# Optimization experiments

Measured on AMD Instinct MI355X. Metric: run time of the kernel, lower is better.

## Reference

```python
import jax, jax.numpy as jnp
import numpy as np

N_AUTHOR, N_PAPER = 20000, 50000
E = 300000
D, H = 256, 8
DK = D // H  # 32


def setup_inputs() -> dict:
    key = jax.random.key(0)
    ks = jax.random.split(key, 20)
    s = np.float32(1.0 / np.sqrt(D))
    sr = np.float32(1.0 / np.sqrt(DK))
    inp = {
        "h_author": jax.random.normal(ks[0], (N_AUTHOR, D), jnp.float32),
        "h_paper": jax.random.normal(ks[1], (N_PAPER, D), jnp.float32),
        "k_w": jax.random.normal(ks[2], (2, D, D), jnp.float32) * s,
        "k_b": jnp.zeros((2, D), jnp.float32),
        "q_w": jax.random.normal(ks[3], (2, D, D), jnp.float32) * s,
        "q_b": jnp.zeros((2, D), jnp.float32),
        "v_w": jax.random.normal(ks[4], (2, D, D), jnp.float32) * s,
        "v_b": jnp.zeros((2, D), jnp.float32),
        "a_w": jax.random.normal(ks[5], (2, D, D), jnp.float32) * s,
        "a_b": jnp.zeros((2, D), jnp.float32),
        "rel_att": jax.random.normal(ks[6], (3, H, DK, DK), jnp.float32) * sr,
        "rel_msg": jax.random.normal(ks[7], (3, H, DK, DK), jnp.float32) * sr,
        "rel_pri": jnp.ones((3, H), jnp.float32),
        "skip": jnp.ones((2,), jnp.float32),
        "src_writes": jax.random.randint(ks[8], (E,), 0, N_AUTHOR),
        "dst_writes": jax.random.randint(ks[9], (E,), 0, N_PAPER),
        "src_cites": jax.random.randint(ks[10], (E,), 0, N_PAPER),
        "dst_cites": jax.random.randint(ks[11], (E,), 0, N_PAPER),
        "src_wb": jax.random.randint(ks[12], (E,), 0, N_PAPER),
        "dst_wb": jax.random.randint(ks[13], (E,), 0, N_AUTHOR),
    }
    return inp


def _seg_softmax(score, seg, n):
    # dst-normalized edge softmax (per-etype subgraph, like DGL edge_softmax)
    m = jax.ops.segment_max(score, seg, num_segments=n)
    m = jnp.where(jnp.isfinite(m), m, 0.0)
    a = jnp.exp(score - m[seg])
    s = jax.ops.segment_sum(a, seg, num_segments=n)
    return a / s[seg]


def _etype_agg(h_src, h_dst, kw, kb, qw, qb, vw, vb, ratt, rmsg, pri, src, dst, n_dst):
    k = (h_src @ kw.T + kb).reshape(-1, H, DK)
    v = (h_src @ vw.T + vb).reshape(-1, H, DK)
    q = (h_dst @ qw.T + qb).reshape(-1, H, DK)
    k = jnp.einsum('nhi,hij->nhj', k, ratt)
    v = jnp.einsum('nhi,hij->nhj', v, rmsg)
    score = (q[dst] * k[src]).sum(-1) * pri / np.float32(np.sqrt(DK))  # [E,H]
    attn = _seg_softmax(score, dst, n_dst)
    return jax.ops.segment_sum(v[src] * attn[:, :, None], dst, num_segments=n_dst)


def reference(h_author, h_paper, k_w, k_b, q_w, q_b, v_w, v_b, a_w, a_b,
              rel_att, rel_msg, rel_pri, skip,
              src_writes, dst_writes, src_cites, dst_cites, src_wb, dst_wb):
    # ntypes: author=0, paper=1; etypes: writes=0 (a->p), cites=1 (p->p), written_by=2 (p->a)
    agg_p = _etype_agg(h_author, h_paper, k_w[0], k_b[0], q_w[1], q_b[1], v_w[0], v_b[0],
                       rel_att[0], rel_msg[0], rel_pri[0], src_writes, dst_writes, N_PAPER)
    agg_p = agg_p + _etype_agg(h_paper, h_paper, k_w[1], k_b[1], q_w[1], q_b[1], v_w[1], v_b[1],
                               rel_att[1], rel_msg[1], rel_pri[1], src_cites, dst_cites, N_PAPER)
    agg_a = _etype_agg(h_paper, h_author, k_w[1], k_b[1], q_w[0], q_b[0], v_w[1], v_b[1],
                       rel_att[2], rel_msg[2], rel_pri[2], src_wb, dst_wb, N_AUTHOR)

    def out_block(agg, h, nid):
        alpha = jax.nn.sigmoid(skip[nid])
        trans = agg.reshape(-1, D) @ a_w[nid].T + a_b[nid]
        return trans * alpha + h * (1.0 - alpha)

    return (out_block(agg_a, h_author, 0), out_block(agg_p, h_paper, 1))
```

## Files before the change

### kernel.cpp

```cpp
#include <hip/hip_runtime.h>
#include <hip/hip_bf16.h>

#define NA 20000
#define NP 50000
#define NE 300000
#define DD 256
#define HH 8
#define NTOT (2 * NP + NA)
#define NBLK ((NTOT + 2047) / 2048)
#define NRT 391

#define CVT_B 8750
#define PREP_B 1792
#define CNT_B 3516
#define PROJ_B (8 * 50 * 14)
#define SCAT_B 3516

typedef short bf16x8 __attribute__((ext_vector_type(8)));
typedef float f32x4 __attribute__((ext_vector_type(4)));

__device__ __forceinline__ float b2f(ushort u) {
  unsigned v = ((unsigned)u) << 16;
  float f;
  __builtin_memcpy(&f, &v, 4);
  return f;
}
__device__ __forceinline__ float b2f_lo(int u) {
  unsigned v = ((unsigned)u) << 16;
  float f;
  __builtin_memcpy(&f, &v, 4);
  return f;
}
__device__ __forceinline__ float b2f_hi(int u) {
  unsigned v = ((unsigned)u) & 0xffff0000u;
  float f;
  __builtin_memcpy(&f, &v, 4);
  return f;
}
__device__ __forceinline__ ushort f2b(float f) {
  unsigned u;
  __builtin_memcpy(&u, &f, 4);
  u = u + 0x7fffu + ((u >> 16) & 1u);
  return (ushort)(u >> 16);
}
__device__ __forceinline__ unsigned pk2(float lo, float hi) {
  return (unsigned)f2b(lo) | ((unsigned)f2b(hi) << 16);
}
__device__ __forceinline__ float ldf(const void* p, int i, int isbf) {
  return isbf ? b2f(((const ushort*)p)[i]) : ((const float*)p)[i];
}
__device__ __forceinline__ int get_isbf(const void* rpri) {
  return ((const unsigned*)rpri)[0] == 0x3F803F80u;
}
__device__ __forceinline__ void gload16(const void* g, void* l) {
  __builtin_amdgcn_global_load_lds(
      (const __attribute__((address_space(1))) void*)g,
      (__attribute__((address_space(3))) void*)l, 16, 0, 0);
}

__global__ __launch_bounds__(256) void phase0(const void* __restrict__ ha,
                                              const void* __restrict__ hp,
                                              ushort* __restrict__ Ha,
                                              ushort* __restrict__ Hp,
                                              const void* __restrict__ q_w,
                                              const void* __restrict__ a_w,
                                              const void* __restrict__ k_w,
                                              const void* __restrict__ v_w,
                                              const void* __restrict__ k_b,
                                              const void* __restrict__ v_b,
                                              const void* __restrict__ q_b,
                                              const void* __restrict__ ratt,
                                              const void* __restrict__ rmsg,
                                              ushort* __restrict__ Bp,
                                              ushort* __restrict__ Ba,
                                              ushort* __restrict__ aeff,
                                              float* __restrict__ gb,
                                              const int* __restrict__ d0,
                                              const int* __restrict__ d1,
                                              const int* __restrict__ d2,
                                              int* __restrict__ cnt,
                                              const void* __restrict__ rpri) {
  const int b = blockIdx.x;
  const int c = threadIdx.x;
  const int isbf = get_isbf(rpri);
  if (b < CVT_B) {
    size_t t = (size_t)b * 256 + c;
    const size_t nA = (size_t)NA * 256 / 8;
    const size_t nT = nA + (size_t)NP * 256 / 8;
    if (t >= nT) return;
    const void* src;
    ushort* dst;
    size_t o;
    if (t < nA) { src = ha; dst = Ha; o = t * 8; }
    else        { src = hp; dst = Hp; o = (t - nA) * 8; }
    if (isbf) {
      *(int4*)(dst + o) = *(const int4*)((const ushort*)src + o);
    } else {
      const float* f = (const float*)src + o;
      float4 x = *(const float4*)f;
      float4 y = *(const float4*)(f + 4);
      int4 v;
      v.x = (int)pk2(x.x, x.y); v.y = (int)pk2(x.z, x.w);
      v.z = (int)pk2(y.x, y.y); v.w = (int)pk2(y.z, y.w);
      *(int4*)(dst + o) = v;
    }
  } else if (b < CVT_B + PREP_B) {
    int pid = b - CVT_B;
    int y = pid >> 8;
    int r = pid & 255;
    if (y < 3) {
      int e = y;
      int nt = (e == 2) ? 0 : 1;
      int h = r >> 5, i = r & 31;
      int rb = ((e * HH + h) * 32 + i) * 32;
      int qb = nt * 65536 + (h * 32) * 256 + c;
      float s = 0.f;
#pragma unroll 8
      for (int j = 0; j < 32; j++) s += ldf(ratt, rb + j, isbf) * ldf(q_w, qb + j * 256, isbf);
      ushort* dst = (e == 2) ? (Ba + (size_t)(512 + r) * 256)
                             : (Bp + (size_t)(512 + e * 256 + r) * 256);
      dst[c] = f2b(s);
    } else if (y < 6) {
      int e = y - 3;
      int o = r;
      int nt = (e == 2) ? 0 : 1;
      int h = c >> 5, i = c & 31;
      int rb = ((e * HH + h) * 32 + i) * 32;
      int ab = nt * 65536 + o * 256 + h * 32;
      float s = 0.f;
#pragma unroll 8
      for (int j = 0; j < 32; j++) s += ldf(rmsg, rb + j, isbf) * ldf(a_w, ab + j, isbf);
      aeff[(e * 256 + o) * 256 + c] = f2b(s);
    } else if (r < 128) {
      int t = r * 256 + c;
      int sec = t >> 13;
      int o = (t & 8191) * 8;
      const void* src = (sec == 0 || sec == 2) ? k_w : v_w;
      size_t soff = (sec < 2) ? (size_t)(65536 + o) : (size_t)o;
      ushort* dst = (sec == 0) ? (Bp + o)
                  : (sec == 1) ? (Bp + 65536 + o)
                  : (sec == 2) ? (Ba + o)
                               : (Ba + 65536 + o);
      if (isbf) {
        *(int4*)dst = *(const int4*)((const ushort*)src + soff);
      } else {
        const float* f = (const float*)src + soff;
        float4 x = *(const float4*)f;
        float4 yy = *(const float4*)(f + 4);
        int4 v;
        v.x = (int)pk2(x.x, x.y); v.y = (int)pk2(x.z, x.w);
        v.z = (int)pk2(yy.x, yy.y); v.w = (int)pk2(yy.z, yy.w);
        *(int4*)dst = v;
      }
    } else if (r == 128) {
      gb[0 * 256 + c] = ldf(k_b, 256 + c, isbf);
      gb[1 * 256 + c] = ldf(v_b, 256 + c, isbf);
      gb[4 * 256 + c] = ldf(k_b, c, isbf);
      gb[5 * 256 + c] = ldf(v_b, c, isbf);
      int h = c >> 5, i = c & 31;
      for (int e = 0; e < 3; e++) {
        int ntp = (e == 2) ? 0 : 1;
        int rb = ((e * HH + h) * 32 + i) * 32;
        float s = 0.f;
        for (int j = 0; j < 32; j++)
          s += ldf(ratt, rb + j, isbf) * ldf(q_b, ntp * 256 + h * 32 + j, isbf);
        gb[(e == 2 ? 6 : (2 + e)) * 256 + c] = s;
      }
    }
  } else {
    int i = (b - CVT_B - PREP_B) * 256 + c;
    if (i >= 3 * NE) return;
    int et = (i >= 2 * NE) ? 2 : ((i >= NE) ? 1 : 0);
    int e = i - et * NE;
    const int* dd = (et == 0) ? d0 : ((et == 1) ? d1 : d2);
    int base = (et == 0) ? 0 : ((et == 1) ? NP : 2 * NP);
    atomicAdd(&cnt[base + dd[e]], 1);
  }
}

struct GemmC4 { ushort* c[4]; int ilv[4]; };

__global__ __launch_bounds__(256) void proj_scatter(const ushort* __restrict__ Hp,
                                                    const ushort* __restrict__ Ha,
                                                    const ushort* __restrict__ Bpp,
                                                    const ushort* __restrict__ Bap,
                                                    const float* __restrict__ gb,
                                                    GemmC4 cpp, GemmC4 cpa,
                                                    const int* __restrict__ s0,
                                                    const int* __restrict__ d0,
                                                    const int* __restrict__ s1,
                                                    const int* __restrict__ d1,
                                                    const int* __restrict__ s2,
                                                    const int* __restrict__ d2,
                                                    int* __restrict__ cur,
                                                    int* __restrict__ csr) {
  __shared__ __align__(16) ushort As[2][4096];
  __shared__ __align__(16) ushort Bs[2][4096];
  const int bid = blockIdx.x;
  if (bid >= PROJ_B) {
    int i = (bid - PROJ_B) * 256 + threadIdx.x;
    if (i >= 3 * NE) return;
    int et = (i >= 2 * NE) ? 2 : ((i >= NE) ? 1 : 0);
    int e = i - et * NE;
    const int* ss = (et == 0) ? s0 : ((et == 1) ? s1 : s2);
    const int* dd = (et == 0) ? d0 : ((et == 1) ? d1 : d2);
    int base = (et == 0) ? 0 : ((et == 1) ? NP : 2 * NP);
    int pos = atomicAdd(&cur[base + dd[e]], 1);
    csr[pos] = ss[e];
    return;
  }
  const int xcd = bid & 7, seq = bid >> 3;
  const int rt = (seq / 14) * 8 + xcd;
  const int y = seq % 14;
  if (rt >= NRT) return;
  const int isNP = (y < 8);
  const int M = isNP ? NP : NA;
  const int row0 = rt * 128;
  if (row0 >= M) return;
  const ushort* A = isNP ? Hp : Ha;
  const ushort* B = isNP ? Bpp : Bap;
  const float* gbias = isNP ? gb : (gb + 1024);
  const int col0 = (isNP ? y : (y - 8)) * 128;
  const GemmC4 cp = isNP ? cpp : cpa;
  ushort* C = cp.c[col0 >> 8];
  const int ilv = cp.ilv[col0 >> 8];
  const int ccol0 = col0 & 255;

  const int tid = threadIdx.x;
  const int ln = tid & 63, wv = tid >> 6;
  const int quad = ln >> 4, lr = ln & 15;
  const int wr = wv >> 1, wc = wv & 1;

  f32x4 acc[4][4];
#pragma unroll
  for (int m = 0; m < 4; m++)
#pragma unroll
    for (int n = 0; n < 4; n++) acc[m][n] = (f32x4){0.f, 0.f, 0.f, 0.f};

  const int r0 = tid >> 2, seg = tid & 3;
  const int r1 = 64 + r0;
  int ar0 = row0 + r0; if (ar0 >= M) ar0 = M - 1;
  int ar1 = row0 + r1; if (ar1 >= M) ar1 = M - 1;
  const ushort* gA0 = A + ((size_t)ar0 * 256 + seg * 8);
  const ushort* gA1 = A + ((size_t)ar1 * 256 + seg * 8);
  const ushort* gB0 = B + ((size_t)(col0 + r0) * 256 + seg * 8);
  const ushort* gB1 = B + ((size_t)(col0 + r1) * 256 + seg * 8);
  const int lbase = (tid & 192) * 8;

  auto stage = [&](int kb, int buf) {
    gload16(gA0 + kb * 32, As[buf] + lbase);
    gload16(gA1 + kb * 32, As[buf] + 2048 + lbase);
    gload16(gB0 + kb * 32, Bs[buf] + lbase);
    gload16(gB1 + kb * 32, Bs[buf] + 2048 + lbase);
  };

  stage(0, 0);
  __syncthreads();
  for (int kb = 0; kb < 8; kb++) {
    const int cur_ = kb & 1;
    if (kb < 7) stage(kb + 1, cur_ ^ 1);
    bf16x8 af[4], bfr[4];
#pragma unroll
    for (int m = 0; m < 4; m++)
      af[m] = *(const bf16x8*)&As[cur_][(wr * 64 + m * 16 + lr) * 32 + quad * 8];
#pragma unroll
    for (int n = 0; n < 4; n++)
      bfr[n] = *(const bf16x8*)&Bs[cur_][(wc * 64 + n * 16 + lr) * 32 + quad * 8];
#pragma unroll
    for (int m = 0; m < 4; m++)
#pragma unroll
      for (int n = 0; n < 4; n++)
        acc[m][n] = __builtin_amdgcn_mfma_f32_16x16x32_bf16(bfr[n], af[m], acc[m][n], 0, 0, 0);
    __syncthreads();
  }

  const int voff = (ilv == 2) ? 4 : 0;
#pragma unroll
  for (int m = 0; m < 4; m++) {
    int row = row0 + wr * 64 + m * 16 + lr;
    if (row >= M) continue;
#pragma unroll
    for (int n = 0; n < 4; n++) {
      int ccol = ccol0 + wc * 64 + n * 16 + quad * 4;
      int gcol = col0 + wc * 64 + n * 16 + quad * 4;
      float4 bv = *(const float4*)(gbias + gcol);
      ushort4 o;
      o.x = f2b(acc[m][n][0] + bv.x);
      o.y = f2b(acc[m][n][1] + bv.y);
      o.z = f2b(acc[m][n][2] + bv.z);
      o.w = f2b(acc[m][n][3] + bv.w);
      size_t cidx = ilv ? ((size_t)row * 512 + (size_t)(ccol >> 2) * 8 + voff)
                        : ((size_t)row * 256 + ccol);
      *(ushort4*)(C + cidx) = o;
    }
  }
}

__global__ __launch_bounds__(256) void out_gemm2(const ushort* __restrict__ Aa,
                                                 const ushort* __restrict__ Ba_,
                                                 const ushort* __restrict__ Ap0,
                                                 const ushort* __restrict__ Bp0,
                                                 const ushort* __restrict__ Ap1,
                                                 const ushort* __restrict__ Bp1,
                                                 const void* __restrict__ ab,
                                                 const void* __restrict__ h_a,
                                                 const void* __restrict__ h_p,
                                                 const void* __restrict__ skipv,
                                                 void* __restrict__ out,
                                                 const void* __restrict__ rpri) {
  const int y = blockIdx.y;
  const int isA = (y < 2);
  const int M = isA ? NA : NP;
  const int row0 = blockIdx.x * 128;
  if (row0 >= M) return;
  const ushort* A0 = isA ? Aa : Ap0;
  const ushort* B0 = isA ? Ba_ : Bp0;
  const ushort* A1 = isA ? nullptr : Ap1;
  const ushort* B1 = isA ? nullptr : Bp1;
  const int ab_off = isA ? 0 : 256;
  const void* h = isA ? h_a : h_p;
  const int skipidx = isA ? 0 : 1;
  const size_t out_off = isA ? 0 : (size_t)NA * DD;
  const int col0 = (isA ? y : (y - 2)) * 128;

  const int isbf = get_isbf(rpri);
  __shared__ __align__(16) ushort As[2][4096];
  __shared__ __align__(16) ushort Bs[2][4096];
  const int tid = threadIdx.x;
  const int ln = tid & 63, wv = tid >> 6;
  const int quad = ln >> 4, lr = ln & 15;
  const int wr = wv >> 1, wc = wv & 1;

  f32x4 acc[4][4];
#pragma unroll
  for (int m = 0; m < 4; m++)
#pragma unroll
    for (int n = 0; n < 4; n++) acc[m][n] = (f32x4){0.f, 0.f, 0.f, 0.f};

  const int r0 = tid >> 2, seg = tid & 3;
  const int r1 = 64 + r0;
  int ar0 = row0 + r0; if (ar0 >= M) ar0 = M - 1;
  int ar1 = row0 + r1; if (ar1 >= M) ar1 = M - 1;
  const int lbase = (tid & 192) * 8;

  const int nsteps = (A1 != nullptr) ? 16 : 8;
  auto stage = [&](int s, int buf) {
    int g = s >> 3, kb = s & 7;
    const ushort* A = g ? A1 : A0;
    const ushort* B = g ? B1 : B0;
    gload16(A + (size_t)ar0 * 256 + seg * 8 + kb * 32, As[buf] + lbase);
    gload16(A + (size_t)ar1 * 256 + seg * 8 + kb * 32, As[buf] + 2048 + lbase);
    gload16(B + (size_t)(col0 + r0) * 256 + seg * 8 + kb * 32, Bs[buf] + lbase);
    gload16(B + (size_t)(col0 + r1) * 256 + seg * 8 + kb * 32, Bs[buf] + 2048 + lbase);
  };

  stage(0, 0);
  __syncthreads();
  for (int s = 0; s < nsteps; s++) {
    const int cur_ = s & 1;
    if (s + 1 < nsteps) stage(s + 1, cur_ ^ 1);
    bf16x8 af[4], bfr[4];
#pragma unroll
    for (int m = 0; m < 4; m++)
      af[m] = *(const bf16x8*)&As[cur_][(wr * 64 + m * 16 + lr) * 32 + quad * 8];
#pragma unroll
    for (int n = 0; n < 4; n++)
      bfr[n] = *(const bf16x8*)&Bs[cur_][(wc * 64 + n * 16 + lr) * 32 + quad * 8];
#pragma unroll
    for (int m = 0; m < 4; m++)
#pragma unroll
      for (int n = 0; n < 4; n++)
        acc[m][n] = __builtin_amdgcn_mfma_f32_16x16x32_bf16(bfr[n], af[m], acc[m][n], 0, 0, 0);
    __syncthreads();
  }

  float alpha = 1.f / (1.f + __expf(-ldf(skipv, skipidx, isbf)));
  float beta = 1.f - alpha;
#pragma unroll
  for (int m = 0; m < 4; m++) {
    int row = row0 + wr * 64 + m * 16 + lr;
    if (row >= M) continue;
#pragma unroll
    for (int n = 0; n < 4; n++) {
      int col = col0 + wc * 64 + n * 16 + quad * 4;
      size_t base = (size_t)row * 256 + col;
      float t0 = acc[m][n][0] + ldf(ab, ab_off + col + 0, isbf);
      float t1 = acc[m][n][1] + ldf(ab, ab_off + col + 1, isbf);
      float t2 = acc[m][n][2] + ldf(ab, ab_off + col + 2, isbf);
      float t3 = acc[m][n][3] + ldf(ab, ab_off + col + 3, isbf);
      if (isbf) {
        ushort4 hu = *(const ushort4*)((const ushort*)h + base);
        ushort4 o;
        o.x = f2b(alpha * t0 + beta * b2f(hu.x));
        o.y = f2b(alpha * t1 + beta * b2f(hu.y));
        o.z = f2b(alpha * t2 + beta * b2f(hu.z));
        o.w = f2b(alpha * t3 + beta * b2f(hu.w));
        *(ushort4*)((ushort*)out + out_off + base) = o;
      } else {
        float4 hf = *(const float4*)((const float*)h + base);
        float4 o;
        o.x = alpha * t0 + beta * hf.x;
        o.y = alpha * t1 + beta * hf.y;
        o.z = alpha * t2 + beta * hf.z;
        o.w = alpha * t3 + beta * hf.w;
        *(float4*)((float*)out + out_off + base) = o;
      }
    }
  }
}

__global__ __launch_bounds__(256) void reduce_cnt(const int* __restrict__ cnt,
                                                  int* __restrict__ bsum) {
  __shared__ int red[256];
  int t = threadIdx.x;
  int base = blockIdx.x * 2048 + t * 8;
  int s = 0;
#pragma unroll
  for (int j = 0; j < 8; j++) s += (base + j < NTOT) ? cnt[base + j] : 0;
  red[t] = s;
  __syncthreads();
  for (int o = 128; o > 0; o >>= 1) {
    if (t < o) red[t] += red[t + o];
    __syncthreads();
  }
  if (t == 0) bsum[blockIdx.x] = red[0];
}

__global__ __launch_bounds__(64) void scan_top(const int* __restrict__ bsum,
                                               int* __restrict__ ebase) {
  __shared__ int ts[64];
  int t = threadIdx.x;
  int v = (t < NBLK) ? bsum[t] : 0;
  ts[t] = v;
  __syncthreads();
  for (int o = 1; o < 64; o <<= 1) {
    int x = (t >= o) ? ts[t - o] : 0;
    __syncthreads();
    ts[t] += x;
    __syncthreads();
  }
  if (t < NBLK) ebase[t] = ts[t] - v;
}

__global__ __launch_bounds__(256) void scan_final(const int* __restrict__ cnt,
                                                  const int* __restrict__ ebase,
                                                  int* __restrict__ offs,
                                                  int* __restrict__ cur) {
  __shared__ int ts[256];
  int t = threadIdx.x;
  int base = blockIdx.x * 2048 + t * 8;
  int v[8];
  int s = 0;
#pragma unroll
  for (int j = 0; j < 8; j++) {
    int x = (base + j < NTOT) ? cnt[base + j] : 0;
    v[j] = s;
    s += x;
  }
  ts[t] = s;
  __syncthreads();
  for (int o = 1; o < 256; o <<= 1) {
    int x = (t >= o) ? ts[t - o] : 0;
    __syncthreads();
    ts[t] += x;
    __syncthreads();
  }
  int tb = ebase[blockIdx.x] + ts[t] - s;
#pragma unroll
  for (int j = 0; j < 8; j++) {
    int i = base + j;
    if (i < NTOT) {
      int o2 = tb + v[j];
      offs[i] = o2;
      cur[i] = o2;
    }
  }
  if (blockIdx.x == 0 && t == 0) offs[NTOT] = 3 * NE;
}

__global__ __launch_bounds__(256) void edge_agg_all(ushort* __restrict__ Qe0,
                                                    ushort* __restrict__ Qe1,
                                                    ushort* __restrict__ Qe2,
                                                    const ushort* __restrict__ KVa,
                                                    const ushort* __restrict__ KVp,
                                                    const int* __restrict__ offs,
                                                    const int* __restrict__ csr,
                                                    const void* __restrict__ pri) {
  int isbf = get_isbf(pri);
  int wv = threadIdx.x >> 6;
  int g = blockIdx.x * 4 + wv;
  if (g >= NTOT) return;
  int ln = threadIdx.x & 63;
  int h = ln >> 3;
  int d, pri_off, n_src;
  ushort* Q;
  const ushort* KV;
  if (g < NP) {
    d = g; Q = Qe0; KV = KVa; pri_off = 0; n_src = NA;
  } else if (g < 2 * NP) {
    d = g - NP; Q = Qe1; KV = KVp; pri_off = 8; n_src = NP;
  } else {
    d = g - 2 * NP; Q = Qe2; KV = KVp; pri_off = 16; n_src = NP;
  }
  float prif = ldf(pri, pri_off + h, isbf) * 0.17677669529663687f;
  ushort4 qu = *(const ushort4*)(Q + (size_t)d * 256 + ln * 4);
  float q0 = b2f(qu.x) * prif, q1 = b2f(qu.y) * prif;
  float q2 = b2f(qu.z) * prif, q3 = b2f(qu.w) * prif;
  float m = -1e30f, l = 0.f;
  float a0 = 0.f, a1 = 0.f, a2 = 0.f, a3 = 0.f;
  int e0 = __builtin_amdgcn_readfirstlane(offs[g]);
  int e1 = __builtin_amdgcn_readfirstlane(offs[g + 1]);
  if (e1 > e0 + 4096) e1 = e0 + 4096;
  const int elast = e1 - 1;

  for (int e = e0; e < e1; e += 8) {
    int nv = e1 - e;
    nv = (nv > 8) ? 8 : nv;
    int4 kv[8];
    float sc[8];
#pragma unroll
    for (int i = 0; i < 8; i++) {
      int idx = e + i;
      idx = (idx > elast) ? elast : idx;
      unsigned s = (unsigned)__builtin_amdgcn_readfirstlane(csr[idx]);
      if (s >= (unsigned)n_src) s = 0;
      kv[i] = *(const int4*)(KV + (size_t)s * 512 + ln * 8);
    }
#pragma unroll
    for (int i = 0; i < 8; i++) {
      float p = q0 * b2f_lo(kv[i].x) + q1 * b2f_hi(kv[i].x) +
                q2 * b2f_lo(kv[i].y) + q3 * b2f_hi(kv[i].y);
      p += __shfl_xor(p, 1);
      p += __shfl_xor(p, 2);
      p += __shfl_xor(p, 4);
      sc[i] = (i < nv) ? p : -1e30f;
    }
    float mc = fmaxf(fmaxf(fmaxf(sc[0], sc[1]), fmaxf(sc[2], sc[3])),
                     fmaxf(fmaxf(sc[4], sc[5]), fmaxf(sc[6], sc[7])));
    float mn = fmaxf(m, mc);
    if (e != e0) {
      float scale = __expf(m - mn);
      l *= scale; a0 *= scale; a1 *= scale; a2 *= scale; a3 *= scale;
    }
#pragma unroll
    for (int i = 0; i < 8; i++) {
      float wgt = __expf(sc[i] - mn);
      l += wgt;
      a0 += wgt * b2f_lo(kv[i].z);
      a1 += wgt * b2f_hi(kv[i].z);
      a2 += wgt * b2f_lo(kv[i].w);
      a3 += wgt * b2f_hi(kv[i].w);
    }
    m = mn;
  }
  float inv = (l > 0.f) ? 1.f / l : 0.f;
  ushort4 o;
  o.x = f2b(a0 * inv);
  o.y = f2b(a1 * inv);
  o.z = f2b(a2 * inv);
  o.w = f2b(a3 * inv);
  *(ushort4*)(Q + (size_t)d * 256 + ln * 4) = o;
}

extern "C" void kernel_launch(void* const* d_in, const int* in_sizes, int n_in,
                              void* d_out, int out_size, void* d_ws, size_t ws_size,
                              hipStream_t stream) {
  (void)in_sizes; (void)n_in; (void)out_size; (void)ws_size;
  const void* h_a = d_in[0];
  const void* h_p = d_in[1];
  const void* k_w = d_in[2];
  const void* k_b = d_in[3];
  const void* q_w = d_in[4];
  const void* q_b = d_in[5];
  const void* v_w = d_in[6];
  const void* v_b = d_in[7];
  const void* a_w = d_in[8];
  const void* a_b = d_in[9];
  const void* ratt = d_in[10];
  const void* rmsg = d_in[11];
  const void* rpri = d_in[12];
  const void* skip = d_in[13];
  const int* src_w = (const int*)d_in[14];
  const int* dst_w = (const int*)d_in[15];
  const int* src_c = (const int*)d_in[16];
  const int* dst_c = (const int*)d_in[17];
  const int* src_b = (const int*)d_in[18];
  const int* dst_b = (const int*)d_in[19];

  char* w = (char*)d_ws;
  size_t ofs = 0;
  auto alloc = [&](size_t bytes) {
    char* p = w + ofs;
    ofs = (ofs + bytes + 255) & ~(size_t)255;
    return p;
  };
  ushort* Bp = (ushort*)alloc((size_t)1024 * 256 * 2);
  ushort* Ba = (ushort*)alloc((size_t)768 * 256 * 2);
  ushort* aeff = (ushort*)alloc((size_t)3 * 256 * 256 * 2);
  float* gb = (float*)alloc((size_t)7 * 256 * 4);
  int* cnt = (int*)alloc((size_t)NTOT * 4);
  int* offs = (int*)alloc((size_t)(NTOT + 1) * 4);
  int* bsum = (int*)alloc(64 * 4);
  int* ebase = (int*)alloc(64 * 4);
  int* cur = (int*)alloc((size_t)NTOT * 4);
  int* csr = (int*)alloc((size_t)3 * NE * 4);
  ushort* Ha = (ushort*)alloc((size_t)NA * DD * 2);
  ushort* Hp = (ushort*)alloc((size_t)NP * DD * 2);
  ushort* KVa = (ushort*)alloc((size_t)NA * 512 * 2);
  ushort* KVp = (ushort*)alloc((size_t)NP * 512 * 2);
  ushort* Qe0 = (ushort*)alloc((size_t)NP * DD * 2);
  ushort* Qe1 = (ushort*)alloc((size_t)NP * DD * 2);
  ushort* Qe2 = (ushort*)alloc((size_t)NA * DD * 2);
  ushort* agg0 = Qe0;
  ushort* agg1 = Qe1;
  ushort* agg2 = Qe2;

  hipMemsetAsync(cnt, 0, (size_t)NTOT * 4, stream);

  phase0<<<CVT_B + PREP_B + CNT_B, 256, 0, stream>>>(
      h_a, h_p, Ha, Hp, q_w, a_w, k_w, v_w, k_b, v_b, q_b, ratt, rmsg,
      Bp, Ba, aeff, gb, dst_w, dst_c, dst_b, cnt, rpri);

  reduce_cnt<<<NBLK, 256, 0, stream>>>(cnt, bsum);
  scan_top<<<1, 64, 0, stream>>>(bsum, ebase);
  scan_final<<<NBLK, 256, 0, stream>>>(cnt, ebase, offs, cur);

  GemmC4 cpp, cpa;
  cpp.c[0] = KVp; cpp.ilv[0] = 1;
  cpp.c[1] = KVp; cpp.ilv[1] = 2;
  cpp.c[2] = Qe0; cpp.ilv[2] = 0;
  cpp.c[3] = Qe1; cpp.ilv[3] = 0;
  cpa.c[0] = KVa; cpa.ilv[0] = 1;
  cpa.c[1] = KVa; cpa.ilv[1] = 2;
  cpa.c[2] = Qe2; cpa.ilv[2] = 0;
  cpa.c[3] = Qe2; cpa.ilv[3] = 0;
  proj_scatter<<<PROJ_B + SCAT_B, 256, 0, stream>>>(
      Hp, Ha, Bp, Ba, gb, cpp, cpa,
      src_w, dst_w, src_c, dst_c, src_b, dst_b, cur, csr);

  edge_agg_all<<<(NTOT + 3) / 4, 256, 0, stream>>>(Qe0, Qe1, Qe2, KVa, KVp,
                                                   offs, csr, rpri);

  out_gemm2<<<dim3((NP + 127) / 128, 4), 256, 0, stream>>>(
      agg2, aeff + 131072, agg0, aeff, agg1, aeff + 65536,
      a_b, h_a, h_p, skip, d_out, rpri);
}
```

Before: 541.6 us.

## Triple-buffer projection GEMM loads and pair K/V columns per output tile

Switches the projection GEMM from double to triple buffering in LDS, with two stages in flight. It uses explicit vmcnt waits and raw barriers in place of __syncthreads, so global loads overlap more MFMA work. It also remaps column tiles so each K/V block computes 64 K columns and the matching 64 V columns, writing complete interleaved KV entries, and replaces the GemmC4 struct with direct pointers. Costs are more LDS per block (possibly lower occupancy) and fragile hand-written wait counts.

```diff
diff --git a/kernel.cpp b/kernel.cpp
--- a/kernel.cpp
+++ b/kernel.cpp
@@ -178,14 +178,16 @@
   }
 }
 
-struct GemmC4 { ushort* c[4]; int ilv[4]; };
-
 __global__ __launch_bounds__(256) void proj_scatter(const ushort* __restrict__ Hp,
                                                     const ushort* __restrict__ Ha,
                                                     const ushort* __restrict__ Bpp,
                                                     const ushort* __restrict__ Bap,
                                                     const float* __restrict__ gb,
-                                                    GemmC4 cpp, GemmC4 cpa,
+                                                    ushort* __restrict__ KVp,
+                                                    ushort* __restrict__ KVa,
+                                                    ushort* __restrict__ Qe0,
+                                                    ushort* __restrict__ Qe1,
+                                                    ushort* __restrict__ Qe2,
                                                     const int* __restrict__ s0,
                                                     const int* __restrict__ d0,
                                                     const int* __restrict__ s1,
@@ -194,8 +196,8 @@
                                                     const int* __restrict__ d2,
                                                     int* __restrict__ cur,
                                                     int* __restrict__ csr) {
-  __shared__ __align__(16) ushort As[2][4096];
-  __shared__ __align__(16) ushort Bs[2][4096];
+  __shared__ __align__(16) ushort As[3][4096];
+  __shared__ __align__(16) ushort Bs[3][4096];
   const int bid = blockIdx.x;
   if (bid >= PROJ_B) {
     int i = (bid - PROJ_B) * 256 + threadIdx.x;
@@ -220,11 +222,28 @@
   const ushort* A = isNP ? Hp : Ha;
   const ushort* B = isNP ? Bpp : Bap;
   const float* gbias = isNP ? gb : (gb + 1024);
-  const int col0 = (isNP ? y : (y - 8)) * 128;
-  const GemmC4 cp = isNP ? cpp : cpa;
-  ushort* C = cp.c[col0 >> 8];
-  const int ilv = cp.ilv[col0 >> 8];
-  const int ccol0 = col0 & 255;
+  const int yy = isNP ? y : (y - 8);
+
+  int pair, c0 = 0, b0, b64, cbias0, cbias64, qcol0 = 0;
+  ushort* Cd;
+  if (yy < 4) {
+    pair = 1;
+    c0 = yy * 64;
+    b0 = c0;
+    b64 = 256 + c0;
+    cbias0 = c0;
+    cbias64 = 192 + c0;
+    Cd = isNP ? KVp : KVa;
+  } else {
+    pair = 0;
+    int j = yy - 4;
+    b0 = 512 + j * 128;
+    b64 = b0 + 64;
+    qcol0 = (j & 1) * 128;
+    cbias0 = 512 + j * 128;
+    cbias64 = cbias0;
+    Cd = isNP ? (j < 2 ? Qe0 : Qe1) : Qe2;
+  }
 
   const int tid = threadIdx.x;
   const int ln = tid & 63, wv = tid >> 6;
@@ -238,13 +257,12 @@
     for (int n = 0; n < 4; n++) acc[m][n] = (f32x4){0.f, 0.f, 0.f, 0.f};
 
   const int r0 = tid >> 2, seg = tid & 3;
-  const int r1 = 64 + r0;
-  int ar0 = row0 + r0; if (ar0 >= M) ar0 = M - 1;
-  int ar1 = row0 + r1; if (ar1 >= M) ar1 = M - 1;
+  int ar0 = row0 + r0;      if (ar0 >= M) ar0 = M - 1;
+  int ar1 = row0 + 64 + r0; if (ar1 >= M) ar1 = M - 1;
   const ushort* gA0 = A + ((size_t)ar0 * 256 + seg * 8);
   const ushort* gA1 = A + ((size_t)ar1 * 256 + seg * 8);
-  const ushort* gB0 = B + ((size_t)(col0 + r0) * 256 + seg * 8);
-  const ushort* gB1 = B + ((size_t)(col0 + r1) * 256 + seg * 8);
+  const ushort* gB0 = B + ((size_t)(b0 + r0) * 256 + seg * 8);
+  const ushort* gB1 = B + ((size_t)(b64 + r0) * 256 + seg * 8);
   const int lbase = (tid & 192) * 8;
 
   auto stage = [&](int kb, int buf) {
@@ -255,10 +273,14 @@
   };
 
   stage(0, 0);
-  __syncthreads();
+  stage(1, 1);
+  asm volatile("s_waitcnt vmcnt(4)" ::: "memory");
+  __builtin_amdgcn_s_barrier();
+  __builtin_amdgcn_sched_barrier(0);
+#pragma unroll
   for (int kb = 0; kb < 8; kb++) {
-    const int cur_ = kb & 1;
-    if (kb < 7) stage(kb + 1, cur_ ^ 1);
+    const int cur_ = kb % 3;
+    if (kb < 6) stage(kb + 2, (kb + 2) % 3);
     bf16x8 af[4], bfr[4];
 #pragma unroll
     for (int m = 0; m < 4; m++)
@@ -271,27 +293,36 @@
 #pragma unroll
       for (int n = 0; n < 4; n++)
         acc[m][n] = __builtin_amdgcn_mfma_f32_16x16x32_bf16(bfr[n], af[m], acc[m][n], 0, 0, 0);
-    __syncthreads();
-  }
-
-  const int voff = (ilv == 2) ? 4 : 0;
+    if (kb < 7) {
+      if (kb < 6) asm volatile("s_waitcnt vmcnt(4)" ::: "memory");
+      else        asm volatile("s_waitcnt vmcnt(0)" ::: "memory");
+      __builtin_amdgcn_s_barrier();
+      __builtin_amdgcn_sched_barrier(0);
+    }
+  }
+
 #pragma unroll
   for (int m = 0; m < 4; m++) {
     int row = row0 + wr * 64 + m * 16 + lr;
     if (row >= M) continue;
 #pragma unroll
     for (int n = 0; n < 4; n++) {
-      int ccol = ccol0 + wc * 64 + n * 16 + quad * 4;
-      int gcol = col0 + wc * 64 + n * 16 + quad * 4;
-      float4 bv = *(const float4*)(gbias + gcol);
+      int lc = wc * 64 + n * 16 + quad * 4;
+      int bidx = ((lc < 64) ? cbias0 : cbias64) + lc;
+      float4 bv = *(const float4*)(gbias + bidx);
       ushort4 o;
       o.x = f2b(acc[m][n][0] + bv.x);
       o.y = f2b(acc[m][n][1] + bv.y);
       o.z = f2b(acc[m][n][2] + bv.z);
       o.w = f2b(acc[m][n][3] + bv.w);
-      size_t cidx = ilv ? ((size_t)row * 512 + (size_t)(ccol >> 2) * 8 + voff)
-                        : ((size_t)row * 256 + ccol);
-      *(ushort4*)(C + cidx) = o;
+      size_t cidx;
+      if (pair) {
+        int dcol = c0 + (lc & 63);
+        cidx = (size_t)row * 512 + (size_t)(dcol >> 2) * 8 + ((lc < 64) ? 0 : 4);
+      } else {
+        cidx = (size_t)row * 256 + qcol0 + lc;
+      }
+      *(ushort4*)(Cd + cidx) = o;
     }
   }
 }
@@ -625,17 +656,8 @@
   scan_top<<<1, 64, 0, stream>>>(bsum, ebase);
   scan_final<<<NBLK, 256, 0, stream>>>(cnt, ebase, offs, cur);
 
-  GemmC4 cpp, cpa;
-  cpp.c[0] = KVp; cpp.ilv[0] = 1;
-  cpp.c[1] = KVp; cpp.ilv[1] = 2;
-  cpp.c[2] = Qe0; cpp.ilv[2] = 0;
-  cpp.c[3] = Qe1; cpp.ilv[3] = 0;
-  cpa.c[0] = KVa; cpa.ilv[0] = 1;
-  cpa.c[1] = KVa; cpa.ilv[1] = 2;
-  cpa.c[2] = Qe2; cpa.ilv[2] = 0;
-  cpa.c[3] = Qe2; cpa.ilv[3] = 0;
   proj_scatter<<<PROJ_B + SCAT_B, 256, 0, stream>>>(
-      Hp, Ha, Bp, Ba, gb, cpp, cpa,
+      Hp, Ha, Bp, Ba, gb, KVp, KVa, Qe0, Qe1, Qe2,
       src_w, dst_w, src_c, dst_c, src_b, dst_b, cur, csr);
 
   edge_agg_all<<<(NTOT + 3) / 4, 256, 0, stream>>>(Qe0, Qe1, Qe2, KVa, KVp,
```

Result: no change. 532.3 us (-1.7%).
